# Kernel tuning notes

Measured on AMD Instinct MI355X. Metric: run time of the kernel, lower is better.

## Reference

```python
import jax, jax.numpy as jnp
import numpy as np

# TrafficXLSTM defaults + xlstm-library internal defaults
D = 128          # embedding_dim
INNER = 256      # mLSTM proj_factor=2 -> inner dim
NH = 4           # mLSTM heads
DHM = INNER // NH
NB = INNER // 4  # qkv_proj_blocksize=4 -> block-diagonal 4x4 blocks
SNH = 4          # sLSTM heads
SDH = D // SNH
FF = 192         # gated FFN up dim: 1.3*128 rounded up to multiple of 64
K = 4            # causal conv kernel size
EPS = 1e-6
BLOCK_TYPES = ['m', 's', 'm', 's', 'm', 'm']  # slstm_at=[1,3], num_blocks=6
B, S, IN_SIZE, OUT_SIZE = 64, 256, 3, 3


def _ln(x, w):  # LayerNorm, weight only (xlstm default bias=False)
    mu = x.mean(-1, keepdims=True)
    var = x.var(-1, keepdims=True)
    return (x - mu) * jax.lax.rsqrt(var + EPS) * w


def _mh_norm(x, w):  # MultiHeadLayerNorm: per-head groupnorm. x: (B,S,NH,dh), w: (NH*dh,)
    mu = x.mean(-1, keepdims=True)
    var = x.var(-1, keepdims=True)
    xn = (x - mu) * jax.lax.rsqrt(var + EPS)
    b, s = x.shape[:2]
    return xn.reshape(b, s, -1) * w


def _causal_conv(x, w, b):  # depthwise causal conv1d. x: (B,S,C), w: (C,K), b: (C,)
    s = x.shape[1]
    xp = jnp.pad(x, ((0, 0), (K - 1, 0), (0, 0)))
    out = b
    for k in range(K):  # fixed small kernel
        out = out + xp[:, k:k + s, :] * w[:, k]
    return out


def _headwise(x, w):  # block-diagonal linear (LinearHeadwiseExpand). x: (B,S,INNER), w: (NB,4,4)
    b, s, _ = x.shape
    xb = x.reshape(b, s, NB, 4)
    return jnp.einsum('bsnk,nkl->bsnl', xb, w).reshape(b, s, -1)


def _mlstm_layer(x, Wup, cw, cb, Wq, Wk, Wv, Wig, big, Wfg, bfg, gnw, skip, Wdown):
    b, s, _ = x.shape
    up = x @ Wup                          # (B,S,2*INNER)
    x_m, z = up[..., :INNER], up[..., INNER:]
    xc = jax.nn.silu(_causal_conv(x_m, cw, cb))
    q = _headwise(xc, Wq)
    k = _headwise(xc, Wk)
    v = _headwise(x_m, Wv)
    qkv = jnp.concatenate([q, k, v], -1)  # gates read concat(q,k,v)
    ig = (qkv @ Wig + big).transpose(0, 2, 1)  # (B,NH,S)
    fg = (qkv @ Wfg + bfg).transpose(0, 2, 1)
    qh = q.reshape(b, s, NH, DHM).transpose(0, 2, 1, 3)  # (B,NH,S,dh)
    kh = k.reshape(b, s, NH, DHM).transpose(0, 2, 1, 3)
    vh = v.reshape(b, s, NH, DHM).transpose(0, 2, 1, 3)
    # parallel stabilized mLSTM (matrix-memory, vanilla backend math)
    logf = jax.nn.log_sigmoid(fg)
    cs = jnp.cumsum(logf, -1)
    logfg = cs[..., :, None] - cs[..., None, :]          # sum_{t=j+1..i} log f_t
    mask = jnp.tril(jnp.ones((s, s), bool))
    logD = jnp.where(mask, logfg + ig[..., None, :], -1e30)
    maxD = logD.max(-1, keepdims=True)
    Dm = jnp.exp(logD - maxD)
    scores = jnp.einsum('bhid,bhjd->bhij', qh, kh) * (DHM ** -0.5)
    C = scores * Dm
    n = jnp.maximum(jnp.abs(C.sum(-1, keepdims=True)), jnp.exp(-maxD)) + EPS
    h = jnp.einsum('bhij,bhjd->bhid', C / n, vh)         # (B,NH,S,dh)
    h = h.transpose(0, 2, 1, 3)                          # (B,S,NH,dh)
    hn = _mh_norm(h, gnw)
    out = (hn + skip * xc) * jax.nn.silu(z)              # learnable skip + output gate
    return out @ Wdown


def _slstm_layer(x, cw, cb, Wg, bg, R, gnw):
    b, s, _ = x.shape
    xc = jax.nn.silu(_causal_conv(x, cw, cb))

    def gate_in(inp, w, bias):  # block-diagonal headwise gate projection
        xb = inp.reshape(b, s, SNH, SDH)
        return jnp.einsum('bsnk,nkl->bsnl', xb, w) + bias.reshape(SNH, SDH)

    gi = gate_in(xc, Wg[0], bg[0])  # i,f gates read conv output
    gf = gate_in(xc, Wg[1], bg[1])
    gz = gate_in(x, Wg[2], bg[2])   # z,o gates read raw input
    go = gate_in(x, Wg[3], bg[3])
    gates = jnp.stack([gi, gf, gz, go], 0)       # (4,B,S,NH,dh)
    gates = jnp.moveaxis(gates, 2, 0)            # (S,4,B,NH,dh)

    def step(carry, g):
        c, n, h, m = carry                       # each (B,NH,dh)
        rec = jnp.einsum('bnk,gnkl->gbnl', h, R)  # block-diag recurrent contribution
        ir, fr = g[0] + rec[0], g[1] + rec[1]
        zr, orr = g[2] + rec[2], g[3] + rec[3]
        mnew = jnp.maximum(fr + m, ir)           # stabilizer state
        i = jnp.exp(ir - mnew)
        f = jnp.exp(fr + m - mnew)
        zt = jnp.tanh(zr)
        o = jax.nn.sigmoid(orr)
        cn = f * c + i * zt
        nn = f * n + i
        hn = o * cn / (nn + 1e-8)
        return (cn, nn, hn, mnew), hn

    z0 = jnp.zeros((b, SNH, SDH), x.dtype)
    _, ys = jax.lax.scan(step, (z0, z0, z0, z0), gates)
    ys = jnp.moveaxis(ys, 0, 1)                  # (B,S,NH,dh)
    return _mh_norm(ys, gnw)


def _ffn(x, Wup, Wdown):  # gated FFN of the sLSTM block
    u = x @ Wup
    g, v = u[..., :FF], u[..., FF:]
    return (jax.nn.gelu(g) * v) @ Wdown


def _forward(x, W_emb, b_emb, m_ln_w, m_Wup, m_conv_w, m_conv_b, m_Wq, m_Wk, m_Wv,
             m_Wig, m_big, m_Wfg, m_bfg, m_gn_w, m_skip, m_Wdown,
             s_ln_w, s_conv_w, s_conv_b, s_Wg, s_bg, s_R, s_gn_w, s_ln2_w,
             s_Wff_up, s_Wff_down, post_ln_w, W_out, b_out):
    h = x @ W_emb + b_emb  # input embedding (dropout = identity in eval)
    mi = si = 0
    for bt in BLOCK_TYPES:
        if bt == 'm':  # mLSTM block: x + mlstm(LN(x))
            h = h + _mlstm_layer(_ln(h, m_ln_w[mi]), m_Wup[mi], m_conv_w[mi], m_conv_b[mi],
                                 m_Wq[mi], m_Wk[mi], m_Wv[mi], m_Wig[mi], m_big[mi],
                                 m_Wfg[mi], m_bfg[mi], m_gn_w[mi], m_skip[mi], m_Wdown[mi])
            mi += 1
        else:          # sLSTM block: x + slstm(LN(x)); x + ffn(LN(x))
            h = h + _slstm_layer(_ln(h, s_ln_w[si]), s_conv_w[si], s_conv_b[si],
                                 s_Wg[si], s_bg[si], s_R[si], s_gn_w[si])
            h = h + _ffn(_ln(h, s_ln2_w[si]), s_Wff_up[si], s_Wff_down[si])
            si += 1
    h = _ln(h, post_ln_w)
    out = h[:, -1, :] @ W_out + b_out
    return out[:, None, :]  # (B, prediction_length=1, output_size)


def setup_inputs() -> dict:
    key = jax.random.key(0)
    ks = iter(jax.random.split(key, 64))

    def w(shape, fan_in):
        return jax.random.normal(next(ks), shape, jnp.float32) / np.sqrt(fan_in)

    nm, ns = 4, 2  # number of mLSTM / sLSTM blocks
    s_bg = jnp.zeros((ns, 4, D)).at[:, 1, :].set(3.0)  # positive forget-gate bias init
    return {
        'x': jax.random.normal(next(ks), (B, S, IN_SIZE), jnp.float32),
        'W_emb': w((IN_SIZE, D), IN_SIZE), 'b_emb': jnp.zeros((D,)),
        'm_ln_w': jnp.ones((nm, D)),
        'm_Wup': w((nm, D, 2 * INNER), D),
        'm_conv_w': w((nm, INNER, K), K), 'm_conv_b': jnp.zeros((nm, INNER)),
        'm_Wq': w((nm, NB, 4, 4), 4), 'm_Wk': w((nm, NB, 4, 4), 4), 'm_Wv': w((nm, NB, 4, 4), 4),
        'm_Wig': w((nm, 3 * INNER, NH), 3 * INNER), 'm_big': jnp.zeros((nm, NH)),
        'm_Wfg': w((nm, 3 * INNER, NH), 3 * INNER),
        'm_bfg': jnp.tile(jnp.linspace(3.0, 6.0, NH), (nm, 1)),
        'm_gn_w': jnp.ones((nm, INNER)), 'm_skip': jnp.ones((nm, INNER)),
        'm_Wdown': w((nm, INNER, D), INNER),
        's_ln_w': jnp.ones((ns, D)),
        's_conv_w': w((ns, D, K), K), 's_conv_b': jnp.zeros((ns, D)),
        's_Wg': w((ns, 4, SNH, SDH, SDH), SDH), 's_bg': s_bg,
        's_R': w((ns, 4, SNH, SDH, SDH), SDH),
        's_gn_w': jnp.ones((ns, D)), 's_ln2_w': jnp.ones((ns, D)),
        's_Wff_up': w((ns, D, 2 * FF), D), 's_Wff_down': w((ns, FF, D), FF),
        'post_ln_w': jnp.ones((D,)),
        'W_out': w((D, OUT_SIZE), D), 'b_out': jnp.zeros((OUT_SIZE,)),
    }


def reference(x, W_emb, b_emb, m_ln_w, m_Wup, m_conv_w, m_conv_b, m_Wq, m_Wk, m_Wv,
              m_Wig, m_big, m_Wfg, m_bfg, m_gn_w, m_skip, m_Wdown,
              s_ln_w, s_conv_w, s_conv_b, s_Wg, s_bg, s_R, s_gn_w, s_ln2_w,
              s_Wff_up, s_Wff_down, post_ln_w, W_out, b_out):
    return _forward(x, W_emb, b_emb, m_ln_w, m_Wup, m_conv_w, m_conv_b, m_Wq, m_Wk, m_Wv,
                    m_Wig, m_big, m_Wfg, m_bfg, m_gn_w, m_skip, m_Wdown,
                    s_ln_w, s_conv_w, s_conv_b, s_Wg, s_bg, s_R, s_gn_w, s_ln2_w,
                    s_Wff_up, s_Wff_down, post_ln_w, W_out, b_out)
```

## Files before the change

kernel.cpp:

```cpp
#include <hip/hip_runtime.h>
#include <hip/hip_bf16.h>

#define D_MODEL 128
#define INNER 256
#define NH 4
#define DHM 64
#define SNH 4
#define SDH 32
#define FF 192
#define CK 4
#define BATCH 64
#define SEQ 256
#define T_TOK (BATCH*SEQ)

typedef __hip_bfloat16 bf16;

__device__ __forceinline__ float sigf(float x){ return 1.0f/(1.0f+__expf(-x)); }
__device__ __forceinline__ float bcast_lane(float v, int k){
    return __uint_as_float(__builtin_amdgcn_readlane(__float_as_uint(v), k));
}
__device__ __forceinline__ float frcp(float x){ return __builtin_amdgcn_rcpf(x); }

__global__ void sentinel_kernel(float* __restrict__ out, float v)
{
    int idx = threadIdx.x;
    if (idx < BATCH*3) out[idx] = v;
}

__global__ void embed_kernel(const float* __restrict__ x, const float* __restrict__ W,
                             const float* __restrict__ bias, float* __restrict__ h)
{
    int idx = blockIdx.x*blockDim.x + threadIdx.x;
    if (idx >= T_TOK*D_MODEL) return;
    int d = idx & 127; int t = idx >> 7;
    float s = bias[d];
    #pragma unroll
    for (int i = 0; i < 3; ++i) s += x[t*3+i] * W[i*D_MODEL+d];
    h[idx] = s;
}

__global__ void ln_kernel(const float* __restrict__ x, const float* __restrict__ w,
                          float* __restrict__ out)
{
    int t = blockIdx.x; int lane = threadIdx.x;
    float v0 = x[(size_t)t*128 + lane], v1 = x[(size_t)t*128 + 64 + lane];
    float s = v0 + v1, ss = v0*v0 + v1*v1;
    #pragma unroll
    for (int off = 32; off >= 1; off >>= 1){ s += __shfl_xor(s,off); ss += __shfl_xor(ss,off); }
    float mu  = s * (1.f/128.f);
    float var = fmaxf(ss * (1.f/128.f) - mu*mu, 0.f);
    float r   = rsqrtf(var + 1e-6f);
    out[(size_t)t*128 + lane]      = (v0-mu)*r*w[lane];
    out[(size_t)t*128 + 64 + lane] = (v1-mu)*r*w[64+lane];
}

#define TM 64
#define TN 64
#define TK 32
__global__ void __launch_bounds__(256)
gemm_tiled_kernel(const float* __restrict__ A, const float* __restrict__ W,
                  float* __restrict__ C, int M, int N, int Kd, int acc)
{
    int ntiles = N / TN;
    int bx = blockIdx.x % ntiles;
    int by = blockIdx.x / ntiles;
    __shared__ float As[TK][TM+1];
    __shared__ float Ws[TK][TN];
    int tid = threadIdx.x;
    int tn = (tid & 15) * 4;
    int tm = (tid >> 4) * 4;
    float accr[4][4] = {{0.f}};
    for (int k0 = 0; k0 < Kd; k0 += TK){
        #pragma unroll
        for (int i = tid; i < TM*TK; i += 256){
            int c2 = i & 31, r = i >> 5;
            As[c2][r] = A[(size_t)(by*TM + r)*Kd + k0 + c2];
        }
        #pragma unroll
        for (int i = tid; i < TK*TN; i += 256){
            int c2 = i & 63, r = i >> 6;
            Ws[r][c2] = W[(size_t)(k0 + r)*N + bx*TN + c2];
        }
        __syncthreads();
        #pragma unroll
        for (int k = 0; k < TK; ++k){
            float a0 = As[k][tm], a1 = As[k][tm+1], a2 = As[k][tm+2], a3 = As[k][tm+3];
            float4 wv = *(const float4*)&Ws[k][tn];
            accr[0][0] = fmaf(a0, wv.x, accr[0][0]); accr[0][1] = fmaf(a0, wv.y, accr[0][1]);
            accr[0][2] = fmaf(a0, wv.z, accr[0][2]); accr[0][3] = fmaf(a0, wv.w, accr[0][3]);
            accr[1][0] = fmaf(a1, wv.x, accr[1][0]); accr[1][1] = fmaf(a1, wv.y, accr[1][1]);
            accr[1][2] = fmaf(a1, wv.z, accr[1][2]); accr[1][3] = fmaf(a1, wv.w, accr[1][3]);
            accr[2][0] = fmaf(a2, wv.x, accr[2][0]); accr[2][1] = fmaf(a2, wv.y, accr[2][1]);
            accr[2][2] = fmaf(a2, wv.z, accr[2][2]); accr[2][3] = fmaf(a2, wv.w, accr[2][3]);
            accr[3][0] = fmaf(a3, wv.x, accr[3][0]); accr[3][1] = fmaf(a3, wv.y, accr[3][1]);
            accr[3][2] = fmaf(a3, wv.z, accr[3][2]); accr[3][3] = fmaf(a3, wv.w, accr[3][3]);
        }
        __syncthreads();
    }
    #pragma unroll
    for (int i = 0; i < 4; ++i){
        size_t off = (size_t)(by*TM + tm + i)*N + bx*TN + tn;
        if (acc){
            float4 old = *(float4*)&C[off];
            old.x += accr[i][0]; old.y += accr[i][1];
            old.z += accr[i][2]; old.w += accr[i][3];
            *(float4*)&C[off] = old;
        } else {
            *(float4*)&C[off] = make_float4(accr[i][0], accr[i][1], accr[i][2], accr[i][3]);
        }
    }
}

__global__ void conv_silu_kernel(const float* __restrict__ in, int istride,
                                 const float* __restrict__ w, const float* __restrict__ bias,
                                 float* __restrict__ out, int C)
{
    int idx = blockIdx.x*blockDim.x + threadIdx.x;
    if (idx >= T_TOK*C) return;
    int c = idx % C; int t = idx / C;
    int s = t & (SEQ-1); int b = t >> 8;
    float a = bias[c];
    int j0 = (s >= CK-1) ? s-(CK-1) : 0;
    for (int j = j0; j <= s; ++j){
        int k = j - s + (CK-1);
        a += in[(size_t)(b*SEQ+j)*istride + c] * w[c*CK + k];
    }
    out[idx] = a * sigf(a);
}

__global__ void headwise_kernel(const float* __restrict__ in, int istride,
                                const float* __restrict__ W, float* __restrict__ out)
{
    int idx = blockIdx.x*blockDim.x + threadIdx.x;
    if (idx >= T_TOK*INNER) return;
    int c = idx & 255; int t = idx >> 8;
    int n = c >> 2, l = c & 3;
    const float* xr = in + (size_t)t*istride + n*4;
    float s = 0.f;
    for (int k = 0; k < 4; ++k) s += xr[k] * W[n*16 + k*4 + l];
    out[idx] = s;
}

__global__ void headwise_inplace_kernel(float* __restrict__ up, const float* __restrict__ W)
{
    int idx = blockIdx.x*blockDim.x + threadIdx.x;
    if (idx >= T_TOK*64) return;
    int n = idx & 63; int t = idx >> 6;
    float* xr = up + (size_t)t*512 + n*4;
    float x0 = xr[0], x1 = xr[1], x2 = xr[2], x3 = xr[3];
    const float* w = W + n*16;
    for (int l = 0; l < 4; ++l)
        xr[l] = x0*w[l] + x1*w[4+l] + x2*w[8+l] + x3*w[12+l];
}

__global__ void __launch_bounds__(256)
gateproj_kernel(const float* __restrict__ q, const float* __restrict__ k,
                const float* __restrict__ up,
                const float* __restrict__ Wig, const float* __restrict__ big,
                const float* __restrict__ Wfg, const float* __restrict__ bfg,
                float* __restrict__ igt, float* __restrict__ fgt)
{
    int t = blockIdx.x*4 + (threadIdx.x >> 6);
    int lane = threadIdx.x & 63;
    float4 si = make_float4(0.f,0.f,0.f,0.f);
    float4 sf = make_float4(0.f,0.f,0.f,0.f);
    #pragma unroll
    for (int c = 0; c < 12; ++c){
        int j = c*64 + lane;
        float xv;
        if (c < 4)      xv = q[(size_t)t*256 + j];
        else if (c < 8) xv = k[(size_t)t*256 + j - 256];
        else            xv = up[(size_t)t*512 + j - 512];
        float4 wi = *(const float4*)(Wig + (size_t)j*4);
        float4 wf = *(const float4*)(Wfg + (size_t)j*4);
        si.x = fmaf(xv, wi.x, si.x); si.y = fmaf(xv, wi.y, si.y);
        si.z = fmaf(xv, wi.z, si.z); si.w = fmaf(xv, wi.w, si.w);
        sf.x = fmaf(xv, wf.x, sf.x); sf.y = fmaf(xv, wf.y, sf.y);
        sf.z = fmaf(xv, wf.z, sf.z); sf.w = fmaf(xv, wf.w, sf.w);
    }
    #pragma unroll
    for (int off = 32; off >= 1; off >>= 1){
        si.x += __shfl_xor(si.x, off); si.y += __shfl_xor(si.y, off);
        si.z += __shfl_xor(si.z, off); si.w += __shfl_xor(si.w, off);
        sf.x += __shfl_xor(sf.x, off); sf.y += __shfl_xor(sf.y, off);
        sf.z += __shfl_xor(sf.z, off); sf.w += __shfl_xor(sf.w, off);
    }
    int b = t >> 8, s = t & 255;
    int hh = lane & 3;
    float vi = (hh==0) ? si.x : (hh==1) ? si.y : (hh==2) ? si.z : si.w;
    float vf = (hh==0) ? sf.x : (hh==1) ? sf.y : (hh==2) ? sf.z : sf.w;
    if (lane < 4)       igt[(b*4+hh)*SEQ + s] = vi + big[hh];
    else if (lane < 8)  fgt[(b*4+hh)*SEQ + s] = vf + bfg[hh];
}

__global__ void __launch_bounds__(64)
cs_kernel(const float* __restrict__ fgt, const float* __restrict__ igt,
          float* __restrict__ cs, float* __restrict__ pm)
{
    int bh = blockIdx.x;
    int lane = threadIdx.x;
    float4 f4 = *(const float4*)(fgt + (size_t)bh*SEQ + lane*4);
    float4 i4 = *(const float4*)(igt + (size_t)bh*SEQ + lane*4);
    float lf0, lf1, lf2, lf3;
    { float f = f4.x; lf0 = (f > 0.f) ? -log1pf(__expf(-f)) : f - log1pf(__expf(f)); }
    { float f = f4.y; lf1 = (f > 0.f) ? -log1pf(__expf(-f)) : f - log1pf(__expf(f)); }
    { float f = f4.z; lf2 = (f > 0.f) ? -log1pf(__expf(-f)) : f - log1pf(__expf(f)); }
    { float f = f4.w; lf3 = (f > 0.f) ? -log1pf(__expf(-f)) : f - log1pf(__expf(f)); }
    float p0 = lf0, p1 = p0 + lf1, p2 = p1 + lf2, p3 = p2 + lf3;
    float incl = p3;
    #pragma unroll
    for (int off = 1; off < 64; off <<= 1){
        float v = __shfl_up(incl, off);
        if (lane >= off) incl += v;
    }
    float excl = __shfl_up(incl, 1);
    if (lane == 0) excl = 0.f;
    float c0 = excl + p0, c1 = excl + p1, c2 = excl + p2, c3 = excl + p3;
    *(float4*)(cs + (size_t)bh*SEQ + lane*4) = make_float4(c0, c1, c2, c3);
    float u0 = i4.x - c0, u1 = i4.y - c1, u2 = i4.z - c2, u3 = i4.w - c3;
    float m0 = u0, m1 = fmaxf(m0, u1), m2 = fmaxf(m1, u2), m3 = fmaxf(m2, u3);
    float inm = m3;
    #pragma unroll
    for (int off = 1; off < 64; off <<= 1){
        float v = __shfl_up(inm, off);
        if (lane >= off) inm = fmaxf(inm, v);
    }
    float exm = __shfl_up(inm, 1);
    if (lane == 0) exm = -1e30f;
    *(float4*)(pm + (size_t)bh*SEQ + lane*4) =
        make_float4(fmaxf(exm, m0), fmaxf(exm, m1), fmaxf(exm, m2), fmaxf(exm, m3));
}

#define AC 32
#define QB 64
__global__ void __launch_bounds__(256)
attn_kernel(float* __restrict__ q, const float* __restrict__ kk,
            const float* __restrict__ up,
            const float* __restrict__ igt, const float* __restrict__ cs,
            const float* __restrict__ pm)
{
    __shared__ float k_sh[AC][DHM];
    __shared__ float v_sh[AC][DHM];
    __shared__ float S_sh[QB][33];
    __shared__ float u_sh[SEQ];
    int blk = blockIdx.x;
    int bh = blk >> 2, qt = blk & 3;
    int b = bh >> 2, hh = bh & 3;
    int tid = threadIdx.x;
    int il = tid & 63;
    int g = tid >> 6;
    int i = qt*QB + il;
    u_sh[tid] = igt[bh*SEQ + tid] - cs[bh*SEQ + tid];
    float csi = cs[bh*SEQ + i];
    float m   = csi + pm[bh*SEQ + i];
    const float4* qp4 = (const float4*)(q + ((size_t)(b*SEQ + i)*INNER + hh*DHM));
    float4 qr4[16];
    #pragma unroll
    for (int r = 0; r < 16; ++r) qr4[r] = qp4[r];
    float4 acc4[4];
    #pragma unroll
    for (int r = 0; r < 4; ++r) acc4[r] = make_float4(0.f,0.f,0.f,0.f);
    float ssum = 0.f;
    int cend = (qt+1)*QB;

    for (int c0 = 0; c0 < cend; c0 += AC){
        {
            int half = tid >> 7;
            int idx2 = tid & 127;
            int r0 = idx2 >> 4;
            int d4 = idx2 & 15;
            #pragma unroll
            for (int rr = 0; rr < 4; ++rr){
                int r = r0 + rr*8;
                size_t tj = (size_t)(b*SEQ + c0 + r);
                if (half == 0)
                    ((float4*)&k_sh[r][0])[d4] = *(const float4*)(kk + tj*INNER + hh*DHM + d4*4);
                else
                    ((float4*)&v_sh[r][0])[d4] = *(const float4*)(up + tj*512 + hh*DHM + d4*4);
            }
        }
        __syncthreads();
        if (i >= c0){
            #pragma unroll
            for (int jj = 0; jj < 8; ++jj){
                int jl = g*8 + jj;
                const float4* kr = (const float4*)&k_sh[jl][0];
                float d0=0.f, d1=0.f, d2=0.f, d3=0.f;
                #pragma unroll
                for (int r4 = 0; r4 < 4; ++r4){
                    float4 ka = kr[r4*4+0], kb2 = kr[r4*4+1];
                    float4 kc = kr[r4*4+2], kd  = kr[r4*4+3];
                    float4 qa = qr4[r4*4+0], qb2 = qr4[r4*4+1];
                    float4 qc = qr4[r4*4+2], qd  = qr4[r4*4+3];
                    d0 += qa.x*ka.x + qa.y*ka.y + qa.z*ka.z + qa.w*ka.w;
                    d1 += qb2.x*kb2.x + qb2.y*kb2.y + qb2.z*kb2.z + qb2.w*kb2.w;
                    d2 += qc.x*kc.x + qc.y*kc.y + qc.z*kc.z + qc.w*kc.w;
                    d3 += qd.x*kd.x + qd.y*kd.y + qd.z*kd.z + qd.w*kd.w;
                }
                float dot = (d0+d1) + (d2+d3);
                int jg = c0 + jl;
                float arg = fminf(csi + u_sh[jg] - m, 0.f);
                S_sh[il][jl] = (jg <= i) ? dot * 0.125f * __expf(arg) : 0.f;
            }
        }
        __syncthreads();
        if (i >= c0){
            #pragma unroll
            for (int jj = 0; jj < AC; ++jj){
                float sv = S_sh[il][jj];
                ssum += sv;
                const float4* vr = (const float4*)&v_sh[jj][g*16];
                #pragma unroll
                for (int r = 0; r < 4; ++r){
                    float4 vv = vr[r];
                    acc4[r].x += sv*vv.x; acc4[r].y += sv*vv.y;
                    acc4[r].z += sv*vv.z; acc4[r].w += sv*vv.w;
                }
            }
        }
        __syncthreads();
    }
    float nrm = fmaxf(fabsf(ssum), __expf(-m)) + 1e-6f;
    float rn = 1.f/nrm;
    float4* op = (float4*)(q + ((size_t)(b*SEQ + i)*INNER + hh*DHM + g*16));
    #pragma unroll
    for (int r = 0; r < 4; ++r){
        float4 o = acc4[r];
        o.x *= rn; o.y *= rn; o.z *= rn; o.w *= rn;
        op[r] = o;
    }
}

__global__ void mh_gate_kernel(float* __restrict__ q, const float* __restrict__ up,
                               const float* __restrict__ xc,
                               const float* __restrict__ gnw, const float* __restrict__ skip)
{
    int idx = blockIdx.x*blockDim.x + threadIdx.x;
    if (idx >= T_TOK*NH) return;
    int hh = idx & 3; int t = idx >> 2;
    float* qp = q + (size_t)t*256 + hh*DHM;
    float s = 0.f;
    for (int d = 0; d < DHM; ++d) s += qp[d];
    float mu = s * (1.f/64.f);
    float v = 0.f;
    for (int d = 0; d < DHM; ++d){ float dv = qp[d]-mu; v += dv*dv; }
    float r = rsqrtf(v * (1.f/64.f) + 1e-6f);
    for (int d = 0; d < DHM; ++d){
        int c = hh*DHM + d;
        float hn = (qp[d]-mu)*r*gnw[c];
        float z  = up[(size_t)t*512 + 256 + c];
        qp[d] = (hn + skip[c]*xc[(size_t)t*256 + c]) * (z*sigf(z));
    }
}

#define SG_TOK 16
__global__ void __launch_bounds__(512)
slstm_gates_kernel(const float* __restrict__ xc, const float* __restrict__ xl,
                   const float* __restrict__ Wg, const float* __restrict__ bg,
                   float* __restrict__ gates)
{
    int tid = threadIdx.x;
    int l  = tid & 31;
    int gn = tid >> 5;
    int g  = gn >> 2, n = gn & 3;
    int t0 = blockIdx.x * SG_TOK;
    float wr[32];
    #pragma unroll
    for (int k = 0; k < 32; ++k) wr[k] = Wg[(size_t)gn*1024 + k*32 + l];
    float bias = bg[g*128 + n*32 + l];
    const float* xin = (g < 2) ? xc : xl;
    #pragma unroll 4
    for (int t = 0; t < SG_TOK; ++t){
        int tok = t0 + t;
        const float4* xr = (const float4*)(xin + (size_t)tok*128 + n*32);
        float a = bias;
        #pragma unroll
        for (int k4 = 0; k4 < 8; ++k4){
            float4 xv = xr[k4];
            a = fmaf(xv.x, wr[k4*4+0], a);
            a = fmaf(xv.y, wr[k4*4+1], a);
            a = fmaf(xv.z, wr[k4*4+2], a);
            a = fmaf(xv.w, wr[k4*4+3], a);
        }
        int b = tok >> 8, s = tok & 255;
        gates[(size_t)((b*4+n)*SEQ + s)*128 + l*4 + g] = a;
    }
}

__global__ void __launch_bounds__(64)
slstm_scan_kernel(const float* __restrict__ gates, const float* __restrict__ Rw,
                  float* __restrict__ ys)
{
    int bn = blockIdx.x;
    int b = bn >> 2, n = bn & 3;
    int lane = threadIdx.x;
    int l = lane & 31;
    int hi = lane >> 5;
    int gA = hi ? 2 : 0, gB = hi ? 3 : 1;
    const float* Rbase = Rw + (size_t)n*1024 + l;
    float Ra[32], Rb[32];
    #pragma unroll
    for (int k = 0; k < 32; ++k){
        Ra[k] = Rbase[(size_t)gA*4096 + k*32];
        Rb[k] = Rbase[(size_t)gB*4096 + k*32];
    }
    const float* gbase = gates + (size_t)bn*SEQ*128 + l*4 + (hi ? 2 : 0);
    float* yrow = ys + (size_t)b*SEQ*128 + n*32 + l;
    float2 g0 = *(const float2*)(gbase);
    float2 g1 = *(const float2*)(gbase + 128);
    float c = 0.f, nst = 0.f, m = 0.f, hst = 0.f;
    for (int s = 0; s < SEQ; ++s){
        float2 g2 = (s+2 < SEQ) ? *(const float2*)(gbase + (size_t)(s+2)*128)
                                : make_float2(0.f, 0.f);
        float ra0=0.f, ra1=0.f, ra2=0.f, ra3=0.f;
        float rb0=0.f, rb1=0.f, rb2=0.f, rb3=0.f;
        #pragma unroll
        for (int k = 0; k < 8; ++k){
            float h0 = bcast_lane(hst, k);
            float h1 = bcast_lane(hst, k+8);
            float h2 = bcast_lane(hst, k+16);
            float h3 = bcast_lane(hst, k+24);
            ra0 = fmaf(h0, Ra[k],    ra0); rb0 = fmaf(h0, Rb[k],    rb0);
            ra1 = fmaf(h1, Ra[k+8],  ra1); rb1 = fmaf(h1, Rb[k+8],  rb1);
            ra2 = fmaf(h2, Ra[k+16], ra2); rb2 = fmaf(h2, Rb[k+16], rb2);
            ra3 = fmaf(h3, Ra[k+24], ra3); rb3 = fmaf(h3, Rb[k+24], rb3);
        }
        float ra = (ra0+ra1) + (ra2+ra3);
        float rb = (rb0+rb1) + (rb2+rb3);
        float pa = g0.x + ra;
        float pb = g0.y + rb;
        float zr  = __shfl_xor(pa, 32);
        float orr = __shfl_xor(pb, 32);
        float mnew = fmaxf(pb + m, pa);
        float iv = __expf(pa - mnew);
        float fv = __expf(pb + m - mnew);
        float zt = 1.f - 2.f*frcp(1.f + __expf(2.f*zr));
        float ov = frcp(1.f + __expf(-orr));
        c   = fv*c + iv*zt;
        nst = fv*nst + iv;
        hst = ov * c * frcp(nst + 1e-8f);
        m = mnew;
        if (!hi) yrow[(size_t)s*128] = hst;
        g0 = g1; g1 = g2;
    }
}

__global__ void mh_add_kernel(const float* __restrict__ ys, const float* __restrict__ gnw,
                              float* __restrict__ h)
{
    int idx = blockIdx.x*blockDim.x + threadIdx.x;
    if (idx >= T_TOK*SNH) return;
    int n = idx & 3; int t = idx >> 2;
    const float* yr = ys + (size_t)t*128 + n*32;
    float s = 0.f;
    for (int l = 0; l < 32; ++l) s += yr[l];
    float mu = s * (1.f/32.f);
    float v = 0.f;
    for (int l = 0; l < 32; ++l){ float dv = yr[l]-mu; v += dv*dv; }
    float r = rsqrtf(v * (1.f/32.f) + 1e-6f);
    for (int l = 0; l < 32; ++l)
        h[(size_t)t*128 + n*32 + l] += (yr[l]-mu)*r*gnw[n*32+l];
}

__global__ void geluv_kernel(const float* __restrict__ up, float* __restrict__ out)
{
    int idx = blockIdx.x*blockDim.x + threadIdx.x;
    if (idx >= T_TOK*FF) return;
    int j = idx % FF; int t = idx / FF;
    float g  = up[(size_t)t*384 + j];
    float vv = up[(size_t)t*384 + FF + j];
    float gel = 0.5f*g*(1.f + tanhf(0.7978845608028654f*(g + 0.044715f*g*g*g)));
    out[idx] = gel*vv;
}

__global__ void out_kernel(const float* __restrict__ ln, const float* __restrict__ W,
                           const float* __restrict__ bias, float* __restrict__ out)
{
    int idx = threadIdx.x;
    if (idx >= BATCH*3) return;
    int b = idx / 3, e = idx % 3;
    float s = bias[e];
    const float* xr = ln + ((size_t)(b*SEQ + SEQ-1))*128;
    for (int d = 0; d < 128; ++d) s += xr[d]*W[d*3+e];
    out[idx] = s;
}

#define LCHK do { \
    if (hipGetLastError() != hipSuccess){ \
        sentinel_kernel<<<1, 192, 0, stream>>>((float*)d_out, 3000.0f + 32.0f*(float)launch_idx); \
        return; } \
    ++launch_idx; } while(0)

extern "C" void kernel_launch(void* const* d_in, const int* in_sizes, int n_in,
                              void* d_out, int out_size, void* d_ws, size_t ws_size,
                              hipStream_t stream)
{
    (void)out_size;
    static const int expected_sizes[30] = {
        49152, 384, 128, 512, 262144, 4096, 1024, 4096, 4096, 4096,
        12288, 16, 12288, 16, 1024, 1024, 131072, 256, 1024, 256,
        32768, 1024, 32768, 256, 256, 98304, 49152, 128, 384, 3
    };
    if (n_in != 30){ sentinel_kernel<<<1,192,0,stream>>>((float*)d_out, 5000.0f); return; }
    for (int i = 0; i < 30; ++i)
        if (in_sizes[i] != expected_sizes[i]){
            sentinel_kernel<<<1,192,0,stream>>>((float*)d_out, 2000.0f + 32.0f*i); return; }
    if (ws_size < (size_t)96*1024*1024){
        sentinel_kernel<<<1,192,0,stream>>>((float*)d_out, 1000.0f + (float)(ws_size >> 20)); return; }

    const float* x        = (const float*)d_in[0];
    const float* W_emb    = (const float*)d_in[1];
    const float* b_emb    = (const float*)d_in[2];
    const float* m_ln_w   = (const float*)d_in[3];
    const float* m_Wup    = (const float*)d_in[4];
    const float* m_conv_w = (const float*)d_in[5];
    const float* m_conv_b = (const float*)d_in[6];
    const float* m_Wq     = (const float*)d_in[7];
    const float* m_Wk     = (const float*)d_in[8];
    const float* m_Wv     = (const float*)d_in[9];
    const float* m_Wig    = (const float*)d_in[10];
    const float* m_big    = (const float*)d_in[11];
    const float* m_Wfg    = (const float*)d_in[12];
    const float* m_bfg    = (const float*)d_in[13];
    const float* m_gn_w   = (const float*)d_in[14];
    const float* m_skip   = (const float*)d_in[15];
    const float* m_Wdown  = (const float*)d_in[16];
    const float* s_ln_w   = (const float*)d_in[17];
    const float* s_conv_w = (const float*)d_in[18];
    const float* s_conv_b = (const float*)d_in[19];
    const float* s_Wg     = (const float*)d_in[20];
    const float* s_bg     = (const float*)d_in[21];
    const float* s_R      = (const float*)d_in[22];
    const float* s_gn_w   = (const float*)d_in[23];
    const float* s_ln2_w  = (const float*)d_in[24];
    const float* s_Wff_up = (const float*)d_in[25];
    const float* s_Wff_dn = (const float*)d_in[26];
    const float* post_ln  = (const float*)d_in[27];
    const float* W_out    = (const float*)d_in[28];
    const float* b_out    = (const float*)d_in[29];

    float* ws  = (float*)d_ws;
    float* h   = ws;
    float* ln  = h   + (size_t)T_TOK*128;
    float* up  = ln  + (size_t)T_TOK*128;
    float* xc  = up  + (size_t)T_TOK*512;
    float* qb  = xc  + (size_t)T_TOK*256;
    float* kb  = qb  + (size_t)T_TOK*256;
    float* igt  = ln;
    float* fgt  = ln + 65536;
    float* csb  = ln + 2*65536;
    float* pmb  = ln + 3*65536;

    int launch_idx = 0;
    (void)hipGetLastError();

    embed_kernel<<<(T_TOK*128)/256, 256, 0, stream>>>(x, W_emb, b_emb, h); LCHK;

    const char* bt = "msmsmm";
    int mi = 0, si = 0;
    for (int blk = 0; blk < 6; ++blk){
        if (bt[blk] == 'm'){
            ln_kernel<<<T_TOK, 64, 0, stream>>>(h, m_ln_w + mi*128, ln); LCHK;
            gemm_tiled_kernel<<<(T_TOK/TM)*(512/TN), 256, 0, stream>>>(ln, m_Wup + (size_t)mi*65536, up, T_TOK, 512, 128, 0); LCHK;
            conv_silu_kernel<<<(T_TOK*256)/256, 256, 0, stream>>>(up, 512, m_conv_w + mi*1024, m_conv_b + mi*256, xc, 256); LCHK;
            headwise_kernel<<<(T_TOK*256)/256, 256, 0, stream>>>(xc, 256, m_Wq + mi*1024, qb); LCHK;
            headwise_kernel<<<(T_TOK*256)/256, 256, 0, stream>>>(xc, 256, m_Wk + mi*1024, kb); LCHK;
            headwise_inplace_kernel<<<(T_TOK*64)/256, 256, 0, stream>>>(up, m_Wv + mi*1024); LCHK;
            gateproj_kernel<<<T_TOK/4, 256, 0, stream>>>(qb, kb, up, m_Wig + mi*3072, m_big + mi*4,
                                                         m_Wfg + mi*3072, m_bfg + mi*4, igt, fgt); LCHK;
            cs_kernel<<<BATCH*NH, 64, 0, stream>>>(fgt, igt, csb, pmb); LCHK;
            attn_kernel<<<BATCH*NH*4, 256, 0, stream>>>(qb, kb, up, igt, csb, pmb); LCHK;
            mh_gate_kernel<<<(T_TOK*4)/256, 256, 0, stream>>>(qb, up, xc, m_gn_w + mi*256, m_skip + mi*256); LCHK;
            gemm_tiled_kernel<<<(T_TOK/TM)*(128/TN), 256, 0, stream>>>(qb, m_Wdown + (size_t)mi*32768, h, T_TOK, 128, 256, 1); LCHK;
            ++mi;
        } else {
            ln_kernel<<<T_TOK, 64, 0, stream>>>(h, s_ln_w + si*128, ln); LCHK;
            conv_silu_kernel<<<(T_TOK*128)/256, 256, 0, stream>>>(ln, 128, s_conv_w + si*512, s_conv_b + si*128, xc, 128); LCHK;
            slstm_gates_kernel<<<T_TOK/SG_TOK, 512, 0, stream>>>(xc, ln, s_Wg + si*16384, s_bg + si*512, up); LCHK;
            slstm_scan_kernel<<<BATCH*4, 64, 0, stream>>>(up, s_R + si*16384, kb); LCHK;
            mh_add_kernel<<<(T_TOK*4)/256, 256, 0, stream>>>(kb, s_gn_w + si*128, h); LCHK;
            ln_kernel<<<T_TOK, 64, 0, stream>>>(h, s_ln2_w + si*128, ln); LCHK;
            gemm_tiled_kernel<<<(T_TOK/TM)*(384/TN), 256, 0, stream>>>(ln, s_Wff_up + (size_t)si*49152, up, T_TOK, 384, 128, 0); LCHK;
            geluv_kernel<<<(T_TOK*192)/256, 256, 0, stream>>>(up, qb); LCHK;
            gemm_tiled_kernel<<<(T_TOK/TM)*(128/TN), 256, 0, stream>>>(qb, s_Wff_dn + (size_t)si*24576, h, T_TOK, 128, 192, 1); LCHK;
            ++si;
        }
    }

    ln_kernel<<<T_TOK, 64, 0, stream>>>(h, post_ln, ln); LCHK;
    out_kernel<<<1, 192, 0, stream>>>(ln, W_out, b_out, (float*)d_out); LCHK;
}
```

Before: 1.876 ms.

## Process two query rows per thread in mLSTM attention to reuse K/V tiles

Result: slower. 3.037 ms (+61.9%).

```diff
diff --git a/kernel.cpp b/kernel.cpp
--- a/kernel.cpp
+++ b/kernel.cpp
@@ -232,7 +232,6 @@
 }
 
 #define AC 32
-#define QB 64
 __global__ void __launch_bounds__(256)
 attn_kernel(float* __restrict__ q, const float* __restrict__ kk,
             const float* __restrict__ up,
@@ -241,27 +240,32 @@
 {
     __shared__ float k_sh[AC][DHM];
     __shared__ float v_sh[AC][DHM];
-    __shared__ float S_sh[QB][33];
+    __shared__ float S_sh[128][33];
     __shared__ float u_sh[SEQ];
     int blk = blockIdx.x;
-    int bh = blk >> 2, qt = blk & 3;
+    int qt = blk >> 8, bh = blk & 255;
     int b = bh >> 2, hh = bh & 3;
     int tid = threadIdx.x;
     int il = tid & 63;
     int g = tid >> 6;
-    int i = qt*QB + il;
+    int iA = qt*128 + il;
+    int iB = iA + 64;
     u_sh[tid] = igt[bh*SEQ + tid] - cs[bh*SEQ + tid];
-    float csi = cs[bh*SEQ + i];
-    float m   = csi + pm[bh*SEQ + i];
-    const float4* qp4 = (const float4*)(q + ((size_t)(b*SEQ + i)*INNER + hh*DHM));
-    float4 qr4[16];
-    #pragma unroll
-    for (int r = 0; r < 16; ++r) qr4[r] = qp4[r];
-    float4 acc4[4];
-    #pragma unroll
-    for (int r = 0; r < 4; ++r) acc4[r] = make_float4(0.f,0.f,0.f,0.f);
-    float ssum = 0.f;
-    int cend = (qt+1)*QB;
+    float csiA = cs[bh*SEQ + iA], mA = csiA + pm[bh*SEQ + iA];
+    float csiB = cs[bh*SEQ + iB], mB = csiB + pm[bh*SEQ + iB];
+    const float4* qpA = (const float4*)(q + ((size_t)(b*SEQ + iA)*INNER + hh*DHM));
+    const float4* qpB = (const float4*)(q + ((size_t)(b*SEQ + iB)*INNER + hh*DHM));
+    float4 qA[16], qB[16];
+    #pragma unroll
+    for (int r = 0; r < 16; ++r){ qA[r] = qpA[r]; qB[r] = qpB[r]; }
+    float4 accA[4], accB[4];
+    #pragma unroll
+    for (int r = 0; r < 4; ++r){
+        accA[r] = make_float4(0.f,0.f,0.f,0.f);
+        accB[r] = make_float4(0.f,0.f,0.f,0.f);
+    }
+    float ssA = 0.f, ssB = 0.f;
+    int cend = (qt+1)*128;
 
     for (int c0 = 0; c0 < cend; c0 += AC){
         {
@@ -280,54 +284,72 @@
             }
         }
         __syncthreads();
-        if (i >= c0){
+        bool doA = (c0 < qt*128 + 64);
+        #pragma unroll
+        for (int jj = 0; jj < 8; ++jj){
+            int jl = g*8 + jj;
+            const float4* kr = (const float4*)&k_sh[jl][0];
+            float a0=0.f, a1=0.f, a2=0.f, a3=0.f;
+            float b0=0.f, b1=0.f, b2=0.f, b3=0.f;
             #pragma unroll
-            for (int jj = 0; jj < 8; ++jj){
-                int jl = g*8 + jj;
-                const float4* kr = (const float4*)&k_sh[jl][0];
-                float d0=0.f, d1=0.f, d2=0.f, d3=0.f;
-                #pragma unroll
-                for (int r4 = 0; r4 < 4; ++r4){
-                    float4 ka = kr[r4*4+0], kb2 = kr[r4*4+1];
-                    float4 kc = kr[r4*4+2], kd  = kr[r4*4+3];
-                    float4 qa = qr4[r4*4+0], qb2 = qr4[r4*4+1];
-                    float4 qc = qr4[r4*4+2], qd  = qr4[r4*4+3];
-                    d0 += qa.x*ka.x + qa.y*ka.y + qa.z*ka.z + qa.w*ka.w;
-                    d1 += qb2.x*kb2.x + qb2.y*kb2.y + qb2.z*kb2.z + qb2.w*kb2.w;
-                    d2 += qc.x*kc.x + qc.y*kc.y + qc.z*kc.z + qc.w*kc.w;
-                    d3 += qd.x*kd.x + qd.y*kd.y + qd.z*kd.z + qd.w*kd.w;
-                }
-                float dot = (d0+d1) + (d2+d3);
-                int jg = c0 + jl;
-                float arg = fminf(csi + u_sh[jg] - m, 0.f);
-                S_sh[il][jl] = (jg <= i) ? dot * 0.125f * __expf(arg) : 0.f;
-            }
-        }
-        __syncthreads();
-        if (i >= c0){
-            #pragma unroll
-            for (int jj = 0; jj < AC; ++jj){
-                float sv = S_sh[il][jj];
-                ssum += sv;
-                const float4* vr = (const float4*)&v_sh[jj][g*16];
-                #pragma unroll
-                for (int r = 0; r < 4; ++r){
-                    float4 vv = vr[r];
-                    acc4[r].x += sv*vv.x; acc4[r].y += sv*vv.y;
-                    acc4[r].z += sv*vv.z; acc4[r].w += sv*vv.w;
+            for (int r4 = 0; r4 < 4; ++r4){
+                float4 ka = kr[r4*4+0], kb2 = kr[r4*4+1];
+                float4 kc = kr[r4*4+2], kd  = kr[r4*4+3];
+                float4 qa = qB[r4*4+0], qb2 = qB[r4*4+1];
+                float4 qc = qB[r4*4+2], qd  = qB[r4*4+3];
+                b0 += qa.x*ka.x + qa.y*ka.y + qa.z*ka.z + qa.w*ka.w;
+                b1 += qb2.x*kb2.x + qb2.y*kb2.y + qb2.z*kb2.z + qb2.w*kb2.w;
+                b2 += qc.x*kc.x + qc.y*kc.y + qc.z*kc.z + qc.w*kc.w;
+                b3 += qd.x*kd.x + qd.y*kd.y + qd.z*kd.z + qd.w*kd.w;
+                if (doA){
+                    float4 pa = qA[r4*4+0], pb2 = qA[r4*4+1];
+                    float4 pc = qA[r4*4+2], pd  = qA[r4*4+3];
+                    a0 += pa.x*ka.x + pa.y*ka.y + pa.z*ka.z + pa.w*ka.w;
+                    a1 += pb2.x*kb2.x + pb2.y*kb2.y + pb2.z*kb2.z + pb2.w*kb2.w;
+                    a2 += pc.x*kc.x + pc.y*kc.y + pc.z*kc.z + pc.w*kc.w;
+                    a3 += pd.x*kd.x + pd.y*kd.y + pd.z*kd.z + pd.w*kd.w;
                 }
             }
+            int jg = c0 + jl;
+            float dotB = (b0+b1) + (b2+b3);
+            float argB = fminf(csiB + u_sh[jg] - mB, 0.f);
+            S_sh[il+64][jl] = (jg <= iB) ? dotB * 0.125f * __expf(argB) : 0.f;
+            if (doA){
+                float dotA = (a0+a1) + (a2+a3);
+                float argA = fminf(csiA + u_sh[jg] - mA, 0.f);
+                S_sh[il][jl] = (jg <= iA) ? dotA * 0.125f * __expf(argA) : 0.f;
+            }
         }
         __syncthreads();
-    }
-    float nrm = fmaxf(fabsf(ssum), __expf(-m)) + 1e-6f;
-    float rn = 1.f/nrm;
-    float4* op = (float4*)(q + ((size_t)(b*SEQ + i)*INNER + hh*DHM + g*16));
+        #pragma unroll
+        for (int jj = 0; jj < AC; ++jj){
+            float svB = S_sh[il+64][jj];
+            float svA = doA ? S_sh[il][jj] : 0.f;
+            ssB += svB; ssA += svA;
+            const float4* vr = (const float4*)&v_sh[jj][g*16];
+            #pragma unroll
+            for (int r = 0; r < 4; ++r){
+                float4 vv = vr[r];
+                accB[r].x += svB*vv.x; accB[r].y += svB*vv.y;
+                accB[r].z += svB*vv.z; accB[r].w += svB*vv.w;
+                accA[r].x += svA*vv.x; accA[r].y += svA*vv.y;
+                accA[r].z += svA*vv.z; accA[r].w += svA*vv.w;
+            }
+        }
+        __syncthreads();
+    }
+    float rnA = 1.f/(fmaxf(fabsf(ssA), __expf(-mA)) + 1e-6f);
+    float rnB = 1.f/(fmaxf(fabsf(ssB), __expf(-mB)) + 1e-6f);
+    float4* opA = (float4*)(q + ((size_t)(b*SEQ + iA)*INNER + hh*DHM + g*16));
+    float4* opB = (float4*)(q + ((size_t)(b*SEQ + iB)*INNER + hh*DHM + g*16));
     #pragma unroll
     for (int r = 0; r < 4; ++r){
-        float4 o = acc4[r];
-        o.x *= rn; o.y *= rn; o.z *= rn; o.w *= rn;
-        op[r] = o;
+        float4 oA = accA[r];
+        oA.x *= rnA; oA.y *= rnA; oA.z *= rnA; oA.w *= rnA;
+        opA[r] = oA;
+        float4 oB = accB[r];
+        oB.x *= rnB; oB.y *= rnB; oB.z *= rnB; oB.w *= rnB;
+        opB[r] = oB;
     }
 }
 
@@ -569,7 +591,7 @@
             gateproj_kernel<<<T_TOK/4, 256, 0, stream>>>(qb, kb, up, m_Wig + mi*3072, m_big + mi*4,
                                                          m_Wfg + mi*3072, m_bfg + mi*4, igt, fgt); LCHK;
             cs_kernel<<<BATCH*NH, 64, 0, stream>>>(fgt, igt, csb, pmb); LCHK;
-            attn_kernel<<<BATCH*NH*4, 256, 0, stream>>>(qb, kb, up, igt, csb, pmb); LCHK;
+            attn_kernel<<<BATCH*NH*2, 256, 0, stream>>>(qb, kb, up, igt, csb, pmb); LCHK;
             mh_gate_kernel<<<(T_TOK*4)/256, 256, 0, stream>>>(qb, up, xc, m_gn_w + mi*256, m_skip + mi*256); LCHK;
             gemm_tiled_kernel<<<(T_TOK/TM)*(128/TN), 256, 0, stream>>>(qb, m_Wdown + (size_t)mi*32768, h, T_TOK, 128, 256, 1); LCHK;
             ++mi;
```
